# Performance work log

Measured on AMD Instinct MI355X. Metric: run time of the kernel, lower is better.

The kernel has to match this reference:

```python
import jax, jax.numpy as jnp
import numpy as np


def setup_inputs() -> dict:
    key = jax.random.key(0)
    k1, k2 = jax.random.split(key)
    B, N, M = 2, 8192, 8192
    source_point_cloud = jax.random.normal(k1, (B, N, 3), dtype=jnp.float32)
    target_point_cloud = jax.random.normal(k2, (B, M, 3), dtype=jnp.float32)
    return {"source_point_cloud": source_point_cloud,
            "target_point_cloud": target_point_cloud}


def reference(source_point_cloud, target_point_cloud):
    # source: [B, N, 3], target: [B, M, 3]
    s, t = source_point_cloud, target_point_cloud
    # Brute-force exact 1-NN (replaces per-batch CPU cKDTree query).
    # ||s - t||^2 = ||s||^2 + ||t||^2 - 2 s.t ; argmin unaffected by const terms per row,
    # but keep ||t||^2 since it varies over the argmin axis.
    s2 = jnp.sum(s * s, axis=-1)                       # [B, N]
    t2 = jnp.sum(t * t, axis=-1)                       # [B, M]
    dots = jnp.einsum('bnd,bmd->bnm', s, t)            # [B, N, M]
    d2 = t2[:, None, :] - 2.0 * dots                   # [B, N, M] (drop s2: row-constant)
    idx = jnp.argmin(d2, axis=-1)                      # [B, N] nearest target index
    target_points = jnp.take_along_axis(t, idx[..., None], axis=1)  # [B, N, 3]
    # MSELoss (mean over all elements) per batch, then mean over batch.
    per_batch = jnp.mean((s - target_points) ** 2, axis=(1, 2))     # [B]
    return jnp.mean(per_batch)
```

## Files before the change

kernel.cpp:

```cpp
#include <hip/hip_runtime.h>

#define BLOCK  256
#define SPL    4
#define TSPLIT 64

typedef float vfloat2 __attribute__((ext_vector_type(2)));
typedef float vfloat4 __attribute__((ext_vector_type(4)));

__device__ __forceinline__ vfloat2 vlo(vfloat4 v) { return __builtin_shufflevector(v, v, 0, 1); }
__device__ __forceinline__ vfloat2 vhi(vfloat4 v) { return __builtin_shufflevector(v, v, 2, 3); }

__global__ __launch_bounds__(256) void prep_kernel(
    const float* __restrict__ tgt, float* __restrict__ soa,
    float* __restrict__ out, int M, int Mp, int BMp)
{
    int i = blockIdx.x * 256 + threadIdx.x;
    if (i == 0) out[0] = 0.f;
    if (i >= BMp) return;
    int b = i / Mp, m = i - b * Mp;
    float x = 0.f, y = 0.f, z = 0.f, w = 1e30f;
    if (m < M) {
        const float* p = tgt + ((size_t)b * M + m) * 3;
        x = p[0]; y = p[1]; z = p[2];
        w = fmaf(x, x, fmaf(y, y, z * z));
    }
    soa[i]           = x;
    soa[BMp + i]     = y;
    soa[2 * BMp + i] = z;
    soa[3 * BMp + i] = w;
}

__global__ __launch_bounds__(BLOCK, 4) void nn_chunk_kernel(
    const float* __restrict__ src, const float* __restrict__ soa,
    float* __restrict__ partial, int N, int Mp, int BMp, int SGB, int BN)
{
    const int tid = threadIdx.x;
    const int c   = blockIdx.x % TSPLIT;
    const int sgg = blockIdx.x / TSPLIT;
    const int b   = sgg / SGB;
    const int sgl = sgg - b * SGB;
    const int si0 = sgl * (BLOCK * SPL) + tid;

    vfloat2 nsx[SPL], nsy[SPL], nsz[SPL];
    float mind[SPL];
#pragma unroll
    for (int s = 0; s < SPL; ++s) {
        const int si = si0 + s * BLOCK;
        float x = 0.f, y = 0.f, z = 0.f;
        if (si < N) {
            const float* p = src + ((size_t)b * N + si) * 3;
            x = p[0]; y = p[1]; z = p[2];
        }
        nsx[s] = {-2.f * x, -2.f * x};
        nsy[s] = {-2.f * y, -2.f * y};
        nsz[s] = {-2.f * z, -2.f * z};
        mind[s] = 1e30f;
    }

    const int CHT = Mp / TSPLIT;
    const int f4  = (b * Mp + c * CHT) >> 2;
    const vfloat4* __restrict__ TX = (const vfloat4*)soa;
    const vfloat4* __restrict__ TY = (const vfloat4*)(soa + BMp);
    const vfloat4* __restrict__ TZ = (const vfloat4*)(soa + 2 * BMp);
    const vfloat4* __restrict__ TW = (const vfloat4*)(soa + 3 * BMp);

#pragma unroll 2
    for (int k = 0; k < CHT / 8; ++k) {
        vfloat4 xa = TX[f4 + 2 * k], xb = TX[f4 + 2 * k + 1];
        vfloat4 ya = TY[f4 + 2 * k], yb = TY[f4 + 2 * k + 1];
        vfloat4 za = TZ[f4 + 2 * k], zb = TZ[f4 + 2 * k + 1];
        vfloat4 wa = TW[f4 + 2 * k], wb = TW[f4 + 2 * k + 1];

#pragma unroll
        for (int s = 0; s < SPL; ++s) {
            vfloat2 d;
            d = __builtin_elementwise_fma(vlo(xa), nsx[s], vlo(wa));
            d = __builtin_elementwise_fma(vlo(ya), nsy[s], d);
            d = __builtin_elementwise_fma(vlo(za), nsz[s], d);
            mind[s] = fminf(mind[s], fminf(d.x, d.y));

            d = __builtin_elementwise_fma(vhi(xa), nsx[s], vhi(wa));
            d = __builtin_elementwise_fma(vhi(ya), nsy[s], d);
            d = __builtin_elementwise_fma(vhi(za), nsz[s], d);
            mind[s] = fminf(mind[s], fminf(d.x, d.y));

            d = __builtin_elementwise_fma(vlo(xb), nsx[s], vlo(wb));
            d = __builtin_elementwise_fma(vlo(yb), nsy[s], d);
            d = __builtin_elementwise_fma(vlo(zb), nsz[s], d);
            mind[s] = fminf(mind[s], fminf(d.x, d.y));

            d = __builtin_elementwise_fma(vhi(xb), nsx[s], vhi(wb));
            d = __builtin_elementwise_fma(vhi(yb), nsy[s], d);
            d = __builtin_elementwise_fma(vhi(zb), nsz[s], d);
            mind[s] = fminf(mind[s], fminf(d.x, d.y));
        }
    }

#pragma unroll
    for (int s = 0; s < SPL; ++s) {
        const int si = si0 + s * BLOCK;
        if (si < N) {
            partial[(size_t)c * BN + (size_t)b * N + si] = mind[s];
        }
    }
}

__global__ __launch_bounds__(BLOCK) void reduce_kernel(
    const float* __restrict__ src, const float* __restrict__ partial,
    float* __restrict__ out, int BN, float scale)
{
    const int i = blockIdx.x * BLOCK + threadIdx.x;
    float v = 0.f;
    if (i < BN) {
        float m0 = 1e30f, m1 = 1e30f, m2 = 1e30f, m3 = 1e30f;
#pragma unroll
        for (int c = 0; c < TSPLIT; c += 4) {
            m0 = fminf(m0, partial[(size_t)(c + 0) * BN + i]);
            m1 = fminf(m1, partial[(size_t)(c + 1) * BN + i]);
            m2 = fminf(m2, partial[(size_t)(c + 2) * BN + i]);
            m3 = fminf(m3, partial[(size_t)(c + 3) * BN + i]);
        }
        float x = src[(size_t)i * 3 + 0];
        float y = src[(size_t)i * 3 + 1];
        float z = src[(size_t)i * 3 + 2];
        v = fmaf(x, x, fmaf(y, y, z * z))
          + fminf(fminf(m0, m1), fminf(m2, m3));
    }

#pragma unroll
    for (int off = 32; off > 0; off >>= 1) v += __shfl_xor(v, off, 64);

    __shared__ float wsum[BLOCK / 64];
    const int lane = threadIdx.x & 63;
    const int w    = threadIdx.x >> 6;
    if (lane == 0) wsum[w] = v;
    __syncthreads();
    if (threadIdx.x == 0) {
        float s = 0.f;
#pragma unroll
        for (int k = 0; k < BLOCK / 64; ++k) s += wsum[k];
        atomicAdd(out, s * scale);
    }
}

extern "C" void kernel_launch(void* const* d_in, const int* in_sizes, int n_in,
                              void* d_out, int out_size, void* d_ws, size_t ws_size,
                              hipStream_t stream) {
    const float* src = (const float*)d_in[0];
    const float* tgt = (const float*)d_in[1];
    float* out = (float*)d_out;

    const int B = 2;
    const int N = in_sizes[0] / (B * 3);
    const int M = in_sizes[1] / (B * 3);
    const int BN = B * N;

    const int step = TSPLIT * 8;
    const int Mp  = ((M + step - 1) / step) * step;
    const int BMp = B * Mp;

    float* soa     = (float*)d_ws;
    float* partial = soa + 4 * (size_t)BMp;

    prep_kernel<<<(BMp + 255) / 256, 256, 0, stream>>>(tgt, soa, out, M, Mp, BMp);

    const int SPB = BLOCK * SPL;
    const int SGB = (N + SPB - 1) / SPB;
    const int grid1 = B * SGB * TSPLIT;
    nn_chunk_kernel<<<grid1, BLOCK, 0, stream>>>(src, soa, partial,
                                                 N, Mp, BMp, SGB, BN);

    reduce_kernel<<<(BN + BLOCK - 1) / BLOCK, BLOCK, 0, stream>>>(
        src, partial, out, BN, 1.0f / (3.0f * (float)N * (float)B));
}
```

Measured before the change: 73.70 us.

## Fuse target prep into NN kernel and stage target chunk in LDS

Removes the separate prep kernel that built an SoA copy of the targets with squared norms. Each NN block now loads its target chunk straight from the AoS input into shared memory, computes the norms there, and then reads the chunk from LDS. This saves one kernel launch and a global round trip. In exchange, each block recomputes norms for its chunk and adds a __syncthreads, and the chunk size is limited by CHT_MAX.

```diff
diff --git a/kernel.cpp b/kernel.cpp
--- a/kernel.cpp
+++ b/kernel.cpp
@@ -1,8 +1,9 @@
 #include <hip/hip_runtime.h>
 
-#define BLOCK  256
-#define SPL    4
-#define TSPLIT 64
+#define BLOCK   256
+#define SPL     4
+#define TSPLIT  64
+#define CHT_MAX 256
 
 typedef float vfloat2 __attribute__((ext_vector_type(2)));
 typedef float vfloat4 __attribute__((ext_vector_type(4)));
@@ -10,29 +11,10 @@
 __device__ __forceinline__ vfloat2 vlo(vfloat4 v) { return __builtin_shufflevector(v, v, 0, 1); }
 __device__ __forceinline__ vfloat2 vhi(vfloat4 v) { return __builtin_shufflevector(v, v, 2, 3); }
 
-__global__ __launch_bounds__(256) void prep_kernel(
-    const float* __restrict__ tgt, float* __restrict__ soa,
-    float* __restrict__ out, int M, int Mp, int BMp)
-{
-    int i = blockIdx.x * 256 + threadIdx.x;
-    if (i == 0) out[0] = 0.f;
-    if (i >= BMp) return;
-    int b = i / Mp, m = i - b * Mp;
-    float x = 0.f, y = 0.f, z = 0.f, w = 1e30f;
-    if (m < M) {
-        const float* p = tgt + ((size_t)b * M + m) * 3;
-        x = p[0]; y = p[1]; z = p[2];
-        w = fmaf(x, x, fmaf(y, y, z * z));
-    }
-    soa[i]           = x;
-    soa[BMp + i]     = y;
-    soa[2 * BMp + i] = z;
-    soa[3 * BMp + i] = w;
-}
-
 __global__ __launch_bounds__(BLOCK, 4) void nn_chunk_kernel(
-    const float* __restrict__ src, const float* __restrict__ soa,
-    float* __restrict__ partial, int N, int Mp, int BMp, int SGB, int BN)
+    const float* __restrict__ src, const float* __restrict__ tgt,
+    float* __restrict__ partial, float* __restrict__ out,
+    int N, int M, int CHT, int SGB, int BN)
 {
     const int tid = threadIdx.x;
     const int c   = blockIdx.x % TSPLIT;
@@ -40,6 +22,23 @@
     const int b   = sgg / SGB;
     const int sgl = sgg - b * SGB;
     const int si0 = sgl * (BLOCK * SPL) + tid;
+
+    if (blockIdx.x == 0 && tid == 0) out[0] = 0.f;
+
+    __shared__ __align__(16) float sxl[CHT_MAX];
+    __shared__ __align__(16) float syl[CHT_MAX];
+    __shared__ __align__(16) float szl[CHT_MAX];
+    __shared__ __align__(16) float swl[CHT_MAX];
+    if (tid < CHT) {
+        const int m = c * CHT + tid;
+        float x = 0.f, y = 0.f, z = 0.f, w = 1e30f;
+        if (m < M) {
+            const float* p = tgt + ((size_t)b * M + m) * 3;
+            x = p[0]; y = p[1]; z = p[2];
+            w = fmaf(x, x, fmaf(y, y, z * z));
+        }
+        sxl[tid] = x; syl[tid] = y; szl[tid] = z; swl[tid] = w;
+    }
 
     vfloat2 nsx[SPL], nsy[SPL], nsz[SPL];
     float mind[SPL];
@@ -57,19 +56,19 @@
         mind[s] = 1e30f;
     }
 
-    const int CHT = Mp / TSPLIT;
-    const int f4  = (b * Mp + c * CHT) >> 2;
-    const vfloat4* __restrict__ TX = (const vfloat4*)soa;
-    const vfloat4* __restrict__ TY = (const vfloat4*)(soa + BMp);
-    const vfloat4* __restrict__ TZ = (const vfloat4*)(soa + 2 * BMp);
-    const vfloat4* __restrict__ TW = (const vfloat4*)(soa + 3 * BMp);
+    __syncthreads();
+
+    const vfloat4* __restrict__ TX = (const vfloat4*)sxl;
+    const vfloat4* __restrict__ TY = (const vfloat4*)syl;
+    const vfloat4* __restrict__ TZ = (const vfloat4*)szl;
+    const vfloat4* __restrict__ TW = (const vfloat4*)swl;
 
 #pragma unroll 2
     for (int k = 0; k < CHT / 8; ++k) {
-        vfloat4 xa = TX[f4 + 2 * k], xb = TX[f4 + 2 * k + 1];
-        vfloat4 ya = TY[f4 + 2 * k], yb = TY[f4 + 2 * k + 1];
-        vfloat4 za = TZ[f4 + 2 * k], zb = TZ[f4 + 2 * k + 1];
-        vfloat4 wa = TW[f4 + 2 * k], wb = TW[f4 + 2 * k + 1];
+        vfloat4 xa = TX[2 * k], xb = TX[2 * k + 1];
+        vfloat4 ya = TY[2 * k], yb = TY[2 * k + 1];
+        vfloat4 za = TZ[2 * k], zb = TZ[2 * k + 1];
+        vfloat4 wa = TW[2 * k], wb = TW[2 * k + 1];
 
 #pragma unroll
         for (int s = 0; s < SPL; ++s) {
@@ -155,20 +154,15 @@
     const int M = in_sizes[1] / (B * 3);
     const int BN = B * N;
 
-    const int step = TSPLIT * 8;
-    const int Mp  = ((M + step - 1) / step) * step;
-    const int BMp = B * Mp;
+    const int CHT = ((M + TSPLIT * 8 - 1) / (TSPLIT * 8)) * 8;
 
-    float* soa     = (float*)d_ws;
-    float* partial = soa + 4 * (size_t)BMp;
-
-    prep_kernel<<<(BMp + 255) / 256, 256, 0, stream>>>(tgt, soa, out, M, Mp, BMp);
+    float* partial = (float*)d_ws;
 
     const int SPB = BLOCK * SPL;
     const int SGB = (N + SPB - 1) / SPB;
     const int grid1 = B * SGB * TSPLIT;
-    nn_chunk_kernel<<<grid1, BLOCK, 0, stream>>>(src, soa, partial,
-                                                 N, Mp, BMp, SGB, BN);
+    nn_chunk_kernel<<<grid1, BLOCK, 0, stream>>>(src, tgt, partial, out,
+                                                 N, M, CHT, SGB, BN);
 
     reduce_kernel<<<(BN + BLOCK - 1) / BLOCK, BLOCK, 0, stream>>>(
         src, partial, out, BN, 1.0f / (3.0f * (float)N * (float)B));
```

After: 70.22 us, median of 2. 4.7% less time.
